# Kernel tuning notes

Measured on AMD Instinct MI355X. Metric: run time of the kernel, lower is better.

Reference implementation:

```python
import jax, jax.numpy as jnp
import numpy as np

H = 1024
N_HEAD = 16
HEAD = H // N_HEAD
EPS = 1e-12


def setup_inputs() -> dict:
    key = jax.random.key(0)
    ks = jax.random.split(key, 12)
    B, S = 2, 2048
    scale = 1.0 / np.sqrt(H)
    inp = {
        "pre_out": jax.random.normal(ks[0], (B, S, H), dtype=jnp.float32),
        "att_mask": jnp.ones((B, 1, 1, S), dtype=jnp.float32),
        "Wq": jax.random.normal(ks[1], (H, H), dtype=jnp.float32) * scale,
        "bq": jnp.zeros((H,), dtype=jnp.float32),
        "Wk": jax.random.normal(ks[2], (H, H), dtype=jnp.float32) * scale,
        "bk": jnp.zeros((H,), dtype=jnp.float32),
        "Wv": jax.random.normal(ks[3], (H, H), dtype=jnp.float32) * scale,
        "bv": jnp.zeros((H,), dtype=jnp.float32),
        "Wo": jax.random.normal(ks[4], (H, H), dtype=jnp.float32) * scale,
        "bo": jnp.zeros((H,), dtype=jnp.float32),
        "ln_w": jnp.ones((H,), dtype=jnp.float32),
        "ln_b": jnp.zeros((H,), dtype=jnp.float32),
    }
    return inp


def _heads(x):
    # [B,S,H] -> [B,n_head,S,head]
    B, S, _ = x.shape
    return x.reshape(B, S, N_HEAD, HEAD).transpose(0, 2, 1, 3)


def _layernorm(x, w, b):
    u = jnp.mean(x, axis=-1, keepdims=True)
    s = jnp.mean((x - u) ** 2, axis=-1, keepdims=True)
    return w * ((x - u) / jnp.sqrt(s + EPS)) + b


def reference(pre_out, att_mask, Wq, bq, Wk, bk, Wv, bv, Wo, bo, ln_w, ln_b):
    B, S, _ = pre_out.shape
    # torch Linear: y = x @ W.T + b
    Q = _heads(pre_out @ Wq.T + bq)
    K = _heads(pre_out @ Wk.T + bk)
    V = _heads(pre_out @ Wv.T + bv)
    scores = jnp.einsum('bhqd,bhkd->bhqk', Q, K) / np.sqrt(HEAD)
    scores = scores + (1.0 - att_mask) * -10000.0
    prob = jax.nn.softmax(scores, axis=-1)  # eval mode: no dropout
    att = jnp.einsum('bhqk,bhkd->bhqd', prob, V)
    att = att.transpose(0, 2, 1, 3).reshape(B, S, H)
    out = att @ Wo.T + bo
    return _layernorm(pre_out + out, ln_w, ln_b)
```

## Files before the change

kernel.cpp:

```cpp
#include <hip/hip_runtime.h>
#include <math.h>

typedef unsigned short u16;
typedef float floatx4 __attribute__((ext_vector_type(4)));
typedef __bf16 bf16x8 __attribute__((ext_vector_type(8)));
typedef u16 u16x4 __attribute__((ext_vector_type(4)));

#define BB 2
#define SS 2048
#define HH 1024
#define NHEAD 16

__device__ __forceinline__ u16 f2bf(float f) {
  union { float f; unsigned u; } a; a.f = f;
  unsigned r = a.u + 0x7fffu + ((a.u >> 16) & 1u);
  return (u16)(r >> 16);
}

__device__ __forceinline__ u16 bfbits(float f) {
  union { __bf16 h; u16 u; } c; c.h = (__bf16)f; return c.u;
}

__device__ __forceinline__ void gload16(const u16* g, u16* l) {
  __builtin_amdgcn_global_load_lds((const __attribute__((address_space(1))) void*)g,
                                   (__attribute__((address_space(3))) void*)l, 16, 0, 0);
}

__device__ __forceinline__ void fencebar() {
  asm volatile("" ::: "memory");
  __builtin_amdgcn_s_barrier();
  asm volatile("" ::: "memory");
}

__global__ __launch_bounds__(256) void cvt_all(
    const float* __restrict__ X, const float* __restrict__ Wq, const float* __restrict__ Wk,
    const float* __restrict__ Wv, const float* __restrict__ Wo, const float* __restrict__ mask,
    u16* __restrict__ Xb, u16* __restrict__ Wqb, u16* __restrict__ Wkb,
    u16* __restrict__ Wvb, u16* __restrict__ Wob, float* __restrict__ B2) {
  int i = blockIdx.x * 256 + threadIdx.x;
  if (i >= (2 << 20)) {
    int off = i - (2 << 20);
    float4 m = ((const float4*)mask)[off];
    float4 o;
    o.x = (1.0f - m.x) * (-10000.0f * 1.44269504f);
    o.y = (1.0f - m.y) * (-10000.0f * 1.44269504f);
    o.z = (1.0f - m.z) * (-10000.0f * 1.44269504f);
    o.w = (1.0f - m.w) * (-10000.0f * 1.44269504f);
    ((float4*)B2)[off] = o;
    return;
  }
  const float* src; u16* dst; int off;
  if (i < (1 << 20)) { src = X; dst = Xb; off = i; }
  else {
    int j = i - (1 << 20);
    int m = j >> 18; off = j & ((1 << 18) - 1);
    src = (m == 0) ? Wq : (m == 1) ? Wk : (m == 2) ? Wv : Wo;
    dst = (m == 0) ? Wqb : (m == 1) ? Wkb : (m == 2) ? Wvb : Wob;
  }
  float4 v = ((const float4*)src)[off];
  u16x4 p; p.x = f2bf(v.x); p.y = f2bf(v.y); p.z = f2bf(v.z); p.w = f2bf(v.w);
  ((u16x4*)dst)[off] = p;
}

__global__ __launch_bounds__(256) void qkv_gemm(
    const u16* __restrict__ X,
    const u16* __restrict__ Wq, const u16* __restrict__ Wk, const u16* __restrict__ Wv,
    const float* __restrict__ bq, const float* __restrict__ bk, const float* __restrict__ bv,
    u16* __restrict__ Qo, u16* __restrict__ Ko, u16* __restrict__ Vt) {
  __shared__ u16 As[2][128 * 32];
  __shared__ u16 Ws[2][128 * 32];

  const int tid = threadIdx.x;
  const int w = tid >> 6, lane = tid & 63, quad = lane >> 4, l15 = lane & 15;
  const int L = blockIdx.y * 24 + blockIdx.x;
  const int wid = (L & 7) * 96 + (L >> 3);
  const int bx = wid % 24, by = wid / 24;
  const int mat = bx >> 3;
  const int col0 = (bx & 7) * 128;
  const int row0 = by * 128;
  const u16* W = (mat == 0) ? Wq : (mat == 1) ? Wk : Wv;
  const float* bias = (mat == 0) ? bq : (mat == 1) ? bk : bv;

  const int c0 = tid, c1 = tid + 256;
  const int ar0 = c0 >> 2, al0 = ((c0 & 3) ^ (ar0 & 3)) * 8;
  const int ar1 = c1 >> 2, al1 = ((c1 & 3) ^ (ar1 & 3)) * 8;
  const u16* gA0 = X + (row0 + ar0) * HH + al0;
  const u16* gA1 = X + (row0 + ar1) * HH + al1;
  const u16* gW0 = W + (col0 + ar0) * HH + al0;
  const u16* gW1 = W + (col0 + ar1) * HH + al1;

  const int wm = (w >> 1) * 64, wn = (w & 1) * 64;
  const int sw = quad ^ (l15 & 3);
  const int aoff = (wm + l15) * 32 + sw * 8;
  const int boff = (wn + l15) * 32 + sw * 8;

  auto stage = [&](int buf, int k0) {
    gload16(gA0 + k0, As[buf] + c0 * 8);
    gload16(gA1 + k0, As[buf] + c1 * 8);
    gload16(gW0 + k0, Ws[buf] + c0 * 8);
    gload16(gW1 + k0, Ws[buf] + c1 * 8);
  };

  floatx4 acc[4][4];
#pragma unroll
  for (int i = 0; i < 4; i++)
#pragma unroll
    for (int j = 0; j < 4; j++) acc[i][j] = {0.f, 0.f, 0.f, 0.f};

  stage(0, 0);

  for (int kt = 0; kt < 32; kt++) {
    const int cur = kt & 1;
    if (kt < 31) {
      stage(cur ^ 1, (kt + 1) * 32);
      asm volatile("s_waitcnt vmcnt(4)" ::: "memory");
    } else {
      asm volatile("s_waitcnt vmcnt(0)" ::: "memory");
    }
    fencebar();

    bf16x8 af[4], bfr[4];
#pragma unroll
    for (int i = 0; i < 4; i++) af[i] = *(const bf16x8*)(As[cur] + aoff + i * 512);
#pragma unroll
    for (int j = 0; j < 4; j++) bfr[j] = *(const bf16x8*)(Ws[cur] + boff + j * 512);
    __builtin_amdgcn_s_setprio(1);
#pragma unroll
    for (int i = 0; i < 4; i++)
#pragma unroll
      for (int j = 0; j < 4; j++)
        acc[i][j] = __builtin_amdgcn_mfma_f32_16x16x32_bf16(af[i], bfr[j], acc[i][j], 0, 0, 0);
    __builtin_amdgcn_s_setprio(0);

    fencebar();
  }

  const int rb = row0 + wm + quad * 4;
  if (mat < 2) {
    u16* O = (mat == 0) ? Qo : Ko;
#pragma unroll
    for (int j = 0; j < 4; j++) {
      const int col = col0 + wn + j * 16 + l15;
      const float bj = bias[col];
#pragma unroll
      for (int i = 0; i < 4; i++) {
        const int r0 = rb + i * 16;
#pragma unroll
        for (int r = 0; r < 4; r++)
          O[(r0 + r) * HH + col] = bfbits(acc[i][j][r] + bj);
      }
    }
  } else {
#pragma unroll
    for (int j = 0; j < 4; j++) {
      const int col = col0 + wn + j * 16 + l15;
      const float bj = bias[col];
      const int h = col >> 6, d = col & 63;
#pragma unroll
      for (int i = 0; i < 4; i++) {
        const int m0 = rb + i * 16;
        const int b = m0 >> 11, s = m0 & 2047;
        u16x4 pk;
#pragma unroll
        for (int r = 0; r < 4; r++) pk[r] = bfbits(acc[i][j][r] + bj);
        *(u16x4*)(Vt + (((b * NHEAD + h) * 64 + d) * SS + s)) = pk;
      }
    }
  }
}

__global__ __launch_bounds__(256) void oproj_gemm(
    const u16* __restrict__ A, const u16* __restrict__ W,
    const float* __restrict__ bias, float* __restrict__ Y) {
  __shared__ u16 As[2][128 * 32];
  __shared__ u16 Ws[2][64 * 32];

  const int tid = threadIdx.x;
  const int w = tid >> 6, lane = tid & 63, quad = lane >> 4, l15 = lane & 15;
  const int L = blockIdx.y * 16 + blockIdx.x;
  const int wid = (L & 7) * 64 + (L >> 3);
  const int col0 = (wid & 15) * 64;
  const int row0 = (wid >> 4) * 128;

  const int c0 = tid, c1 = tid + 256;
  const int ar0 = c0 >> 2, al0 = ((c0 & 3) ^ (ar0 & 3)) * 8;
  const int ar1 = c1 >> 2, al1 = ((c1 & 3) ^ (ar1 & 3)) * 8;
  const u16* gA0 = A + (row0 + ar0) * HH + al0;
  const u16* gA1 = A + (row0 + ar1) * HH + al1;
  const u16* gW0 = W + (col0 + ar0) * HH + al0;

  const int wm = w * 32;
  const int sw = quad ^ (l15 & 3);
  const int aoff = (wm + l15) * 32 + sw * 8;
  const int boff = l15 * 32 + sw * 8;

  auto stage = [&](int buf, int k0) {
    gload16(gA0 + k0, As[buf] + c0 * 8);
    gload16(gA1 + k0, As[buf] + c1 * 8);
    gload16(gW0 + k0, Ws[buf] + c0 * 8);
  };

  floatx4 acc[2][4];
#pragma unroll
  for (int i = 0; i < 2; i++)
#pragma unroll
    for (int j = 0; j < 4; j++) acc[i][j] = {0.f, 0.f, 0.f, 0.f};

  stage(0, 0);

  for (int kt = 0; kt < 32; kt++) {
    const int cur = kt & 1;
    if (kt < 31) {
      stage(cur ^ 1, (kt + 1) * 32);
      asm volatile("s_waitcnt vmcnt(3)" ::: "memory");
    } else {
      asm volatile("s_waitcnt vmcnt(0)" ::: "memory");
    }
    fencebar();

    bf16x8 af[2], bfr[4];
#pragma unroll
    for (int i = 0; i < 2; i++) af[i] = *(const bf16x8*)(As[cur] + aoff + i * 512);
#pragma unroll
    for (int j = 0; j < 4; j++) bfr[j] = *(const bf16x8*)(Ws[cur] + boff + j * 512);
    __builtin_amdgcn_s_setprio(1);
#pragma unroll
    for (int i = 0; i < 2; i++)
#pragma unroll
      for (int j = 0; j < 4; j++)
        acc[i][j] = __builtin_amdgcn_mfma_f32_16x16x32_bf16(af[i], bfr[j], acc[i][j], 0, 0, 0);
    __builtin_amdgcn_s_setprio(0);

    fencebar();
  }

  const int rb = row0 + wm + quad * 4;
#pragma unroll
  for (int j = 0; j < 4; j++) {
    const int col = col0 + j * 16 + l15;
    const float bj = bias[col];
#pragma unroll
    for (int i = 0; i < 2; i++) {
      const int r0 = rb + i * 16;
#pragma unroll
      for (int r = 0; r < 4; r++)
        Y[(r0 + r) * HH + col] = acc[i][j][r] + bj;
    }
  }
}

#define QT 128

__global__ __launch_bounds__(512, 4) void attn_mfma(
    const u16* __restrict__ Q, const u16* __restrict__ K, const u16* __restrict__ Vt,
    const float* __restrict__ B2, u16* __restrict__ O) {
  __shared__ u16 SMEM[26624];
  u16* const UQ = SMEM;
  u16* const KS0 = SMEM + 10240;
  u16* const KS1 = SMEM + 14336;
  u16* const VS0 = SMEM + 18432;
  u16* const VS1 = SMEM + 22528;

  const int L = blockIdx.y * 16 + blockIdx.x;
  const int wid = (L & 7) * 64 + (L >> 3);
  const int qt = wid & 15, bh = wid >> 4;
  const int b = bh >> 4, h = bh & 15;
  const int tid = threadIdx.x;
  const int w = tid >> 6, lane = tid & 63, quad = lane >> 4, l15 = lane & 15;
  const int sw = l15 & 7;
  const int qg = w & 3;
  const int khalf = w >> 2;
  const int koff = khalf * 32;
  const int kh4 = khalf * 4;

  const int qbase  = (b * SS + qt * QT) * HH + h * 64;
  const int kvbase = (b * SS) * HH + h * 64;
  const int vtbase = (b * NHEAD + h) * 64 * SS;

  auto stage_kv = [&](u16* kd, u16* vd, int t) {
    const int c = tid;
    const int r = c >> 3, lc = (c & 7) ^ (r & 7);
    gload16(K + kvbase + (t * 64 + r) * HH + lc * 8, kd + c * 8);
    gload16(Vt + vtbase + r * SS + t * 64 + lc * 8, vd + c * 8);
  };

#pragma unroll
  for (int i = 0; i < 2; i++) {
    const int c = tid + i * 512;
    const int r = c >> 3, lc = (c & 7) ^ (r & 7);
    gload16(Q + qbase + r * HH + lc * 8, UQ + c * 8);
  }
  stage_kv(KS0, VS0, 0);
  asm volatile("s_waitcnt vmcnt(2)" ::: "memory");
  fencebar();

  bf16x8 aQ[2][2];
#pragma unroll
  for (int mt = 0; mt < 2; mt++) {
    const u16* qr = UQ + (qg * 32 + mt * 16 + l15) * 64;
    aQ[mt][0] = *(const bf16x8*)(qr + ((quad ^ sw) * 8));
    aQ[mt][1] = *(const bf16x8*)(qr + (((4 + quad) ^ sw) * 8));
  }
  asm volatile("s_waitcnt lgkmcnt(0)" ::: "memory");

  floatx4 o[2][4];
#pragma unroll
  for (int mt = 0; mt < 2; mt++)
#pragma unroll
    for (int j = 0; j < 4; j++) o[mt][j] = {0.f, 0.f, 0.f, 0.f};
  float lp[2] = {0.f, 0.f};

  u16* const Pw = UQ + w * 1280;
  const float* B2row = B2 + b * SS;

  for (int kt = 0; kt < 32; kt++) {
    const int cur = kt & 1;
    const u16* Kc = cur ? KS1 : KS0;
    const u16* Vc = cur ? VS1 : VS0;

    const float* B2k = B2row + kt * 64 + koff;
    floatx4 bb[2];
    bb[0] = *(const floatx4*)(B2k + quad * 4);
    bb[1] = *(const floatx4*)(B2k + 16 + quad * 4);
    asm volatile("" ::: "memory");

    if (kt < 31) {
      stage_kv(cur ? KS0 : KS1, cur ? VS0 : VS1, kt + 1);
      asm volatile("s_waitcnt vmcnt(2)" ::: "memory");
    } else {
      asm volatile("s_waitcnt vmcnt(0)" ::: "memory");
    }
    fencebar();

    floatx4 st[2][2];
    __builtin_amdgcn_s_setprio(1);
#pragma unroll
    for (int kb = 0; kb < 2; kb++) {
      const u16* kr = Kc + (koff + kb * 16 + l15) * 64;
      bf16x8 kf0 = *(const bf16x8*)(kr + ((quad ^ sw) * 8));
      bf16x8 kf1 = *(const bf16x8*)(kr + (((4 + quad) ^ sw) * 8));
#pragma unroll
      for (int mt = 0; mt < 2; mt++) {
        floatx4 z = {0.f, 0.f, 0.f, 0.f};
        z = __builtin_amdgcn_mfma_f32_16x16x32_bf16(kf0, aQ[mt][0], z, 0, 0, 0);
        st[mt][kb] = __builtin_amdgcn_mfma_f32_16x16x32_bf16(kf1, aQ[mt][1], z, 0, 0, 0);
      }
    }
    __builtin_amdgcn_s_setprio(0);

#pragma unroll
    for (int kb = 0; kb < 2; kb++) {
#pragma unroll
      for (int mt = 0; mt < 2; mt++) {
        u16x4 pk;
#pragma unroll
        for (int r = 0; r < 4; r++) {
          const float p = __builtin_amdgcn_exp2f(st[mt][kb][r] * 0.180336880f + bb[kb][r]);
          lp[mt] += p;
          pk[r] = bfbits(p);
        }
        *(u16x4*)(Pw + (mt * 16 + l15) * 40 + kb * 16 + quad * 4) = pk;
      }
    }

    bf16x8 pa[2];
#pragma unroll
    for (int mt = 0; mt < 2; mt++)
      pa[mt] = *(const bf16x8*)(Pw + (mt * 16 + l15) * 40 + quad * 8);
    __builtin_amdgcn_s_setprio(1);
#pragma unroll
    for (int j = 0; j < 4; j++) {
      const u16* vr = Vc + (j * 16 + l15) * 64;
      bf16x8 vf = *(const bf16x8*)(vr + (((kh4 + quad) ^ sw) * 8));
#pragma unroll
      for (int mt = 0; mt < 2; mt++)
        o[mt][j] = __builtin_amdgcn_mfma_f32_16x16x32_bf16(pa[mt], vf, o[mt][j], 0, 0, 0);
    }
    __builtin_amdgcn_s_setprio(0);

    fencebar();
  }

#pragma unroll
  for (int mt = 0; mt < 2; mt++) {
    float v = lp[mt];
    v += __shfl_xor(v, 16);
    v += __shfl_xor(v, 32);
    lp[mt] = v;
  }

  float* const oS  = (float*)(SMEM + 10240);
  float* const lpS = (float*)SMEM;
  if (w >= 4) {
    float* pb = oS + (w - 4) * 2048;
#pragma unroll
    for (int mt = 0; mt < 2; mt++) {
#pragma unroll
      for (int j = 0; j < 4; j++)
#pragma unroll
        for (int r = 0; r < 4; r++)
          pb[(mt * 16 + quad * 4 + r) * 64 + j * 16 + l15] = o[mt][j][r];
      if (quad == 0) lpS[qg * 32 + mt * 16 + l15] = lp[mt];
    }
  }
  asm volatile("s_waitcnt lgkmcnt(0)" ::: "memory");
  fencebar();

  if (w < 4) {
    const float* pb = oS + w * 2048;
    float lpt[2];
#pragma unroll
    for (int mt = 0; mt < 2; mt++)
      lpt[mt] = lp[mt] + lpS[w * 32 + mt * 16 + l15];
#pragma unroll
    for (int mt = 0; mt < 2; mt++) {
      const int orow0 = b * SS + qt * QT + qg * 32 + mt * 16 + quad * 4;
#pragma unroll
      for (int r = 0; r < 4; r++) {
        const float inv = 1.0f / __shfl(lpt[mt], quad * 4 + r);
#pragma unroll
        for (int j = 0; j < 4; j++) {
          const float val = o[mt][j][r] + pb[(mt * 16 + quad * 4 + r) * 64 + j * 16 + l15];
          O[(orow0 + r) * HH + h * 64 + j * 16 + l15] = bfbits(val * inv);
        }
      }
    }
  }
}

__device__ __forceinline__ float block_sum256(float v) {
  __shared__ float sb[4];
#pragma unroll
  for (int o = 1; o < 64; o <<= 1) v += __shfl_xor(v, o);
  if ((threadIdx.x & 63) == 0) sb[threadIdx.x >> 6] = v;
  __syncthreads();
  float r = sb[0] + sb[1] + sb[2] + sb[3];
  __syncthreads();
  return r;
}

__global__ __launch_bounds__(256) void add_layernorm(
    const float* __restrict__ x0, const float* __restrict__ y,
    const float* __restrict__ w, const float* __restrict__ b,
    float* __restrict__ out) {
  const int row = blockIdx.x;
  const int t = threadIdx.x;
  const float* xr = x0 + (size_t)row * HH;
  const float* yr = y + (size_t)row * HH;

  float v[4];
  float sum = 0.f;
#pragma unroll
  for (int i = 0; i < 4; i++) {
    int idx = t + i * 256;
    v[i] = xr[idx] + yr[idx];
    sum += v[i];
  }
  float mean = block_sum256(sum) * (1.0f / HH);

  float sq = 0.f;
#pragma unroll
  for (int i = 0; i < 4; i++) {
    float d = v[i] - mean;
    sq += d * d;
  }
  float var = block_sum256(sq) * (1.0f / HH);
  float inv = rsqrtf(var + 1e-12f);

#pragma unroll
  for (int i = 0; i < 4; i++) {
    int idx = t + i * 256;
    out[(size_t)row * HH + idx] = w[idx] * ((v[i] - mean) * inv) + b[idx];
  }
}

extern "C" void kernel_launch(void* const* d_in, const int* in_sizes, int n_in,
                              void* d_out, int out_size, void* d_ws, size_t ws_size,
                              hipStream_t stream) {
  const float* pre_out = (const float*)d_in[0];
  const float* mask    = (const float*)d_in[1];
  const float* Wq = (const float*)d_in[2];
  const float* bq = (const float*)d_in[3];
  const float* Wk = (const float*)d_in[4];
  const float* bk = (const float*)d_in[5];
  const float* Wv = (const float*)d_in[6];
  const float* bv = (const float*)d_in[7];
  const float* Wo = (const float*)d_in[8];
  const float* bo = (const float*)d_in[9];
  const float* ln_w = (const float*)d_in[10];
  const float* ln_b = (const float*)d_in[11];
  float* out = (float*)d_out;

  u16* Xb  = (u16*)d_ws;
  u16* Wqb = Xb + (4 << 20);
  u16* Wkb = Wqb + (1 << 20);
  u16* Wvb = Wkb + (1 << 20);
  u16* Wob = Wvb + (1 << 20);
  u16* Qb  = Wob + (1 << 20);
  u16* Kb  = Qb + (4 << 20);
  u16* Vtb = Kb + (4 << 20);
  u16* Ab  = Vtb + (4 << 20);
  float* Yb = (float*)(Ab + (4 << 20));
  float* B2 = Yb + (4 << 20);

  cvt_all<<<8196, 256, 0, stream>>>(pre_out, Wq, Wk, Wv, Wo, mask,
                                    Xb, Wqb, Wkb, Wvb, Wob, B2);

  qkv_gemm<<<dim3(24, 32), 256, 0, stream>>>(Xb, Wqb, Wkb, Wvb, bq, bk, bv, Qb, Kb, Vtb);

  attn_mfma<<<dim3(SS / QT, BB * NHEAD), 512, 0, stream>>>(Qb, Kb, Vtb, B2, Ab);

  oproj_gemm<<<dim3(16, 32), 256, 0, stream>>>(Ab, Wob, bo, Yb);

  add_layernorm<<<BB * SS, 256, 0, stream>>>(pre_out, Yb, ln_w, ln_b, out);
}
```

Before: 208.9 us.

## Triple-buffer K/V tiles in attention and use one wave per row in layernorm

The attention kernel moves from a double-buffered to a triple-buffered K/V LDS ring. Tiles are prefetched two steps ahead, and one of the two block barriers per iteration is dropped, so global loads overlap more with compute. The add+layernorm kernel now gives one 64-lane wave to each row, using float4 loads and stores and wave-shuffle reductions with no LDS or block syncs. In exchange, attention LDS use grows by about 16KB per block, which may reduce occupancy at the 4-blocks launch bound.

```diff
diff --git a/kernel.cpp b/kernel.cpp
--- a/kernel.cpp
+++ b/kernel.cpp
@@ -254,12 +254,10 @@
 __global__ __launch_bounds__(512, 4) void attn_mfma(
     const u16* __restrict__ Q, const u16* __restrict__ K, const u16* __restrict__ Vt,
     const float* __restrict__ B2, u16* __restrict__ O) {
-  __shared__ u16 SMEM[26624];
+  __shared__ u16 SMEM[34816];
   u16* const UQ = SMEM;
-  u16* const KS0 = SMEM + 10240;
-  u16* const KS1 = SMEM + 14336;
-  u16* const VS0 = SMEM + 18432;
-  u16* const VS1 = SMEM + 22528;
+  u16* const KB = SMEM + 10240;
+  u16* const VB = SMEM + 22528;
 
   const int L = blockIdx.y * 16 + blockIdx.x;
   const int wid = (L & 7) * 64 + (L >> 3);
@@ -277,11 +275,11 @@
   const int kvbase = (b * SS) * HH + h * 64;
   const int vtbase = (b * NHEAD + h) * 64 * SS;
 
-  auto stage_kv = [&](u16* kd, u16* vd, int t) {
+  auto stage_kv = [&](int bi, int t) {
     const int c = tid;
     const int r = c >> 3, lc = (c & 7) ^ (r & 7);
-    gload16(K + kvbase + (t * 64 + r) * HH + lc * 8, kd + c * 8);
-    gload16(Vt + vtbase + r * SS + t * 64 + lc * 8, vd + c * 8);
+    gload16(K + kvbase + (t * 64 + r) * HH + lc * 8, KB + bi * 4096 + c * 8);
+    gload16(Vt + vtbase + r * SS + t * 64 + lc * 8, VB + bi * 4096 + c * 8);
   };
 
 #pragma unroll
@@ -290,8 +288,9 @@
     const int r = c >> 3, lc = (c & 7) ^ (r & 7);
     gload16(Q + qbase + r * HH + lc * 8, UQ + c * 8);
   }
-  stage_kv(KS0, VS0, 0);
-  asm volatile("s_waitcnt vmcnt(2)" ::: "memory");
+  stage_kv(0, 0);
+  stage_kv(1, 1);
+  asm volatile("s_waitcnt vmcnt(4)" ::: "memory");
   fencebar();
 
   bf16x8 aQ[2][2];
@@ -314,9 +313,9 @@
   const float* B2row = B2 + b * SS;
 
   for (int kt = 0; kt < 32; kt++) {
-    const int cur = kt & 1;
-    const u16* Kc = cur ? KS1 : KS0;
-    const u16* Vc = cur ? VS1 : VS0;
+    const int cI = kt % 3;
+
+    fencebar();
 
     const float* B2k = B2row + kt * 64 + koff;
     floatx4 bb[2];
@@ -324,13 +323,15 @@
     bb[1] = *(const floatx4*)(B2k + 16 + quad * 4);
     asm volatile("" ::: "memory");
 
-    if (kt < 31) {
-      stage_kv(cur ? KS0 : KS1, cur ? VS0 : VS1, kt + 1);
+    if (kt < 30) {
+      stage_kv((kt + 2) % 3, kt + 2);
       asm volatile("s_waitcnt vmcnt(2)" ::: "memory");
     } else {
       asm volatile("s_waitcnt vmcnt(0)" ::: "memory");
     }
-    fencebar();
+
+    const u16* Kc = KB + cI * 4096;
+    const u16* Vc = VB + cI * 4096;
 
     floatx4 st[2][2];
     __builtin_amdgcn_s_setprio(1);
@@ -377,9 +378,9 @@
         o[mt][j] = __builtin_amdgcn_mfma_f32_16x16x32_bf16(pa[mt], vf, o[mt][j], 0, 0, 0);
     }
     __builtin_amdgcn_s_setprio(0);
-
-    fencebar();
-  }
+  }
+
+  fencebar();
 
 #pragma unroll
   for (int mt = 0; mt < 2; mt++) {
@@ -428,49 +429,51 @@
   }
 }
 
-__device__ __forceinline__ float block_sum256(float v) {
-  __shared__ float sb[4];
-#pragma unroll
-  for (int o = 1; o < 64; o <<= 1) v += __shfl_xor(v, o);
-  if ((threadIdx.x & 63) == 0) sb[threadIdx.x >> 6] = v;
-  __syncthreads();
-  float r = sb[0] + sb[1] + sb[2] + sb[3];
-  __syncthreads();
-  return r;
-}
-
 __global__ __launch_bounds__(256) void add_layernorm(
     const float* __restrict__ x0, const float* __restrict__ y,
     const float* __restrict__ w, const float* __restrict__ b,
     float* __restrict__ out) {
-  const int row = blockIdx.x;
-  const int t = threadIdx.x;
-  const float* xr = x0 + (size_t)row * HH;
-  const float* yr = y + (size_t)row * HH;
-
-  float v[4];
-  float sum = 0.f;
+  const int row = blockIdx.x * 4 + (threadIdx.x >> 6);
+  const int l = threadIdx.x & 63;
+  const float4* xr = (const float4*)(x0 + (size_t)row * HH);
+  const float4* yr = (const float4*)(y + (size_t)row * HH);
+
+  float4 v[4];
+  float s = 0.f;
 #pragma unroll
   for (int i = 0; i < 4; i++) {
-    int idx = t + i * 256;
-    v[i] = xr[idx] + yr[idx];
-    sum += v[i];
-  }
-  float mean = block_sum256(sum) * (1.0f / HH);
+    const float4 a = xr[l + i * 64];
+    const float4 c = yr[l + i * 64];
+    v[i].x = a.x + c.x; v[i].y = a.y + c.y;
+    v[i].z = a.z + c.z; v[i].w = a.w + c.w;
+    s += v[i].x + v[i].y + v[i].z + v[i].w;
+  }
+#pragma unroll
+  for (int o = 1; o < 64; o <<= 1) s += __shfl_xor(s, o);
+  const float mean = s * (1.0f / HH);
 
   float sq = 0.f;
 #pragma unroll
   for (int i = 0; i < 4; i++) {
-    float d = v[i] - mean;
-    sq += d * d;
-  }
-  float var = block_sum256(sq) * (1.0f / HH);
-  float inv = rsqrtf(var + 1e-12f);
-
+    const float dx = v[i].x - mean, dy = v[i].y - mean;
+    const float dz = v[i].z - mean, dw = v[i].w - mean;
+    sq += dx * dx + dy * dy + dz * dz + dw * dw;
+  }
+#pragma unroll
+  for (int o = 1; o < 64; o <<= 1) sq += __shfl_xor(sq, o);
+  const float inv = rsqrtf(sq * (1.0f / HH) + 1e-12f);
+
+  float4* orow = (float4*)(out + (size_t)row * HH);
 #pragma unroll
   for (int i = 0; i < 4; i++) {
-    int idx = t + i * 256;
-    out[(size_t)row * HH + idx] = w[idx] * ((v[i] - mean) * inv) + b[idx];
+    const float4 ww = ((const float4*)w)[l + i * 64];
+    const float4 bb = ((const float4*)b)[l + i * 64];
+    float4 o4;
+    o4.x = ww.x * ((v[i].x - mean) * inv) + bb.x;
+    o4.y = ww.y * ((v[i].y - mean) * inv) + bb.y;
+    o4.z = ww.z * ((v[i].z - mean) * inv) + bb.z;
+    o4.w = ww.w * ((v[i].w - mean) * inv) + bb.w;
+    orow[l + i * 64] = o4;
   }
 }
 
@@ -512,5 +515,5 @@
 
   oproj_gemm<<<dim3(16, 32), 256, 0, stream>>>(Ab, Wob, bo, Yb);
 
-  add_layernorm<<<BB * SS, 256, 0, stream>>>(pre_out, Yb, ln_w, ln_b, out);
-}
+  add_layernorm<<<BB * SS / 4, 256, 0, stream>>>(pre_out, Yb, ln_w, ln_b, out);
+}
```

After: 206.6 us. No clear change (-1.1%).
